# Optimization experiments

Hardware: AMD Instinct MI355X
Metric: run time of the kernel (lower is better)

The kernel has to match this reference:

```python
import jax, jax.numpy as jnp
import numpy as np

D_MODEL = 512
HEADS = 8
CTX = 2048
BATCH = 4
SEQ = 2048


def make_rotary_matrix(context_window, d):
    # Faithful to the source, including theta = 10000 ** (-2*(i-1)/d)
    i = np.arange(d // 2)
    theta = 10000.0 ** (-2.0 * (i - 1) / d)  # [d/2]
    pos = np.arange(context_window)
    m_theta = pos[:, None] * theta[None, :]  # [m, d/2]
    cos, sin = np.cos(m_theta), np.sin(m_theta)
    R = np.zeros((context_window, d, d), dtype=np.float32)
    even, odd = 2 * i, 2 * i + 1
    R[:, even, even] = cos
    R[:, even, odd] = -sin
    R[:, odd, even] = sin
    R[:, odd, odd] = cos
    return jnp.asarray(R)


def setup_inputs() -> dict:
    key = jax.random.key(0)
    ks = jax.random.split(key, 8)
    s = 1.0 / np.sqrt(D_MODEL)
    x = jax.random.normal(ks[0], (BATCH, SEQ, D_MODEL), dtype=jnp.float32)
    Wq = jax.random.normal(ks[1], (D_MODEL, D_MODEL), dtype=jnp.float32) * s
    Wk = jax.random.normal(ks[2], (D_MODEL, D_MODEL), dtype=jnp.float32) * s
    Wv = jax.random.normal(ks[3], (D_MODEL, D_MODEL), dtype=jnp.float32) * s
    in_proj_w = jax.random.normal(ks[4], (3 * D_MODEL, D_MODEL), dtype=jnp.float32) * s
    in_proj_b = jax.random.normal(ks[5], (3 * D_MODEL,), dtype=jnp.float32) * 0.01
    out_w = jax.random.normal(ks[6], (D_MODEL, D_MODEL), dtype=jnp.float32) * s
    out_b = jax.random.normal(ks[7], (D_MODEL,), dtype=jnp.float32) * 0.01
    R = make_rotary_matrix(CTX, D_MODEL)
    return {"x": x, "Wq": Wq, "Wk": Wk, "Wv": Wv, "R": R,
            "in_proj_w": in_proj_w, "in_proj_b": in_proj_b,
            "out_w": out_w, "out_b": out_b}


def reference(x, Wq, Wk, Wv, R, in_proj_w, in_proj_b, out_w, out_b):
    b, m, d = x.shape
    h = HEADS
    hd = d // h
    # outer QKV projections (bias=False)
    q = x @ Wq.T
    k = x @ Wk.T
    v = x @ Wv.T
    # dense per-position rotary rotation: q_out[b,p,:] = q[b,p,:] @ R[p]
    Rm = R[:m]
    q = jnp.einsum('bmd,mde->bme', q, Rm)
    k = jnp.einsum('bmd,mde->bme', k, Rm)
    v = jnp.einsum('bmd,mde->bme', v, Rm)
    # nn.MultiheadAttention in_proj (bias=True) -- dropout skipped (eval)
    wq_i, wk_i, wv_i = jnp.split(in_proj_w, 3, axis=0)
    bq, bk, bv = jnp.split(in_proj_b, 3, axis=0)
    qp = (q @ wq_i.T + bq).reshape(b, m, h, hd).transpose(0, 2, 1, 3)
    kp = (k @ wk_i.T + bk).reshape(b, m, h, hd).transpose(0, 2, 1, 3)
    vp = (v @ wv_i.T + bv).reshape(b, m, h, hd).transpose(0, 2, 1, 3)
    scale = 1.0 / np.sqrt(hd)
    scores = jnp.einsum('bhqd,bhkd->bhqk', qp, kp) * scale
    causal = jnp.triu(jnp.full((m, m), -jnp.inf, dtype=scores.dtype), k=1)
    attn = jax.nn.softmax(scores + causal, axis=-1)
    out = jnp.einsum('bhqk,bhkd->bhqd', attn, vp)
    out = out.transpose(0, 2, 1, 3).reshape(b, m, d)
    return out @ out_w.T + out_b
```

## Files before the change

### kernel.cpp

```cpp
#include <hip/hip_runtime.h>
#include <cmath>

typedef unsigned short u16;
typedef __bf16 bf16x8 __attribute__((ext_vector_type(8)));
typedef float f32x4 __attribute__((ext_vector_type(4)));

#define SEQL 2048
#define NH 8
#define HD 64
#define MROWS 8192

typedef __attribute__((address_space(1))) unsigned int gu32;
typedef __attribute__((address_space(3))) unsigned int lu32;

static __device__ __forceinline__ u16 f2bf(float f) {
  union { float f; unsigned u; } v; v.f = f;
  unsigned u = v.u;
  unsigned r = (u + 0x7FFFu + ((u >> 16) & 1u)) >> 16;
  return (u16)r;
}

static __device__ __forceinline__ void gl16(const u16* g, u16* l) {
  __builtin_amdgcn_global_load_lds((const gu32*)g, (lu32*)l, 16, 0, 0);
}

template<int ROWS>
static __device__ __forceinline__ void stage_tile(const u16* __restrict__ gt, int ld,
                                                  u16* lds, int wid, int lane) {
  int rowl = lane >> 3;
  int coff = ((lane & 7) ^ rowl) * 8;
  #pragma unroll
  for (int t = 0; t < ROWS / 32; ++t) {
    int grp = t * 4 + wid;
    gl16(gt + (size_t)(grp * 8 + rowl) * ld + coff, lds + grp * 512);
  }
}

static __device__ __forceinline__ void cvt4(const float* __restrict__ in,
                                            u16* __restrict__ out, int lb) {
  int i = lb * 1024 + threadIdx.x * 4;
  float4 f = *(const float4*)(in + i);
  ushort4 o;
  o.x = f2bf(f.x); o.y = f2bf(f.y); o.z = f2bf(f.z); o.w = f2bf(f.w);
  *(ushort4*)(out + i) = o;
}

__global__ __launch_bounds__(256) void prep_kernel(
    const float* __restrict__ x,  const float* __restrict__ Wq,
    const float* __restrict__ Wk, const float* __restrict__ Wv,
    const float* __restrict__ ipw, const float* __restrict__ ow,
    u16* __restrict__ xb, u16* __restrict__ Wcatb, u16* __restrict__ ipwb,
    u16* __restrict__ owb, float2* __restrict__ T) {
  int b = blockIdx.x;
  if (b < 4096)      cvt4(x,   xb,                 b);
  else if (b < 4352) cvt4(Wq,  Wcatb,              b - 4096);
  else if (b < 4608) cvt4(Wk,  Wcatb + 262144,     b - 4352);
  else if (b < 4864) cvt4(Wv,  Wcatb + 524288,     b - 4608);
  else if (b < 5632) cvt4(ipw, ipwb,               b - 4864);
  else if (b < 5888) cvt4(ow,  owb,                b - 5632);
  else {
    int idx = (b - 5888) * 256 + threadIdx.x;
    int m = idx >> 8, i = idx & 255;
    double theta = pow(10000.0, -2.0 * ((double)i - 1.0) / 512.0);
    double a = (double)m * theta;
    T[idx] = make_float2((float)cos(a), (float)sin(a));
  }
}

template<int MODE>
__global__ __launch_bounds__(256) void gemm_bt(const u16* __restrict__ A, int lda,
                                               const u16* __restrict__ B, int ldb,
                                               const float* __restrict__ bias,
                                               void* __restrict__ Cv, int ldc,
                                               const float2* __restrict__ T) {
  __shared__ u16 As[128 * 64];
  __shared__ u16 Bs[128 * 64];
  int tid = threadIdx.x;
  int wid = tid >> 6, lane = tid & 63, quad = lane >> 4, l16 = lane & 15;
  int x7 = l16 & 7;
  int m0 = blockIdx.y * 128, n0 = blockIdx.x * 128;
  int wm = (wid >> 1) * 64, wn = (wid & 1) * 64;
  f32x4 acc[4][4] = {};
  for (int kb = 0; kb < 512; kb += 64) {
    stage_tile<128>(A + (size_t)m0 * lda + kb, lda, As, wid, lane);
    stage_tile<128>(B + (size_t)n0 * ldb + kb, ldb, Bs, wid, lane);
    __syncthreads();
    #pragma unroll
    for (int kk = 0; kk < 2; ++kk) {
      int sw = ((kk * 4 + quad) ^ x7) * 8;
      bf16x8 af[4], bfr[4];
      #pragma unroll
      for (int i = 0; i < 4; ++i)
        af[i] = *(const bf16x8*)(&As[(wm + 16 * i + l16) * 64 + sw]);
      #pragma unroll
      for (int j = 0; j < 4; ++j)
        bfr[j] = *(const bf16x8*)(&Bs[(wn + 16 * j + l16) * 64 + sw]);
      #pragma unroll
      for (int i = 0; i < 4; ++i)
        #pragma unroll
        for (int j = 0; j < 4; ++j)
          acc[i][j] = __builtin_amdgcn_mfma_f32_16x16x32_bf16(af[i], bfr[j], acc[i][j], 0, 0, 0);
    }
    __syncthreads();
  }
  float sgn = (l16 & 1) ? -1.f : 1.f;
  #pragma unroll
  for (int i = 0; i < 4; ++i)
    #pragma unroll
    for (int j = 0; j < 4; ++j)
      #pragma unroll
      for (int r = 0; r < 4; ++r) {
        int row = m0 + wm + 16 * i + quad * 4 + r;
        int col = n0 + wn + 16 * j + l16;
        float v = acc[i][j][r];
        if (MODE == 3) {
          float partner = __shfl_xor(v, 1, 64);
          float2 cs = T[(row & 2047) * 256 + ((col & 511) >> 1)];
          v = v * cs.x + sgn * partner * cs.y;
          ((u16*)Cv)[(size_t)row * ldc + col] = f2bf(v);
        } else {
          v += bias[col];
          ((float*)Cv)[(size_t)row * ldc + col] = v;
        }
      }
}

__global__ __launch_bounds__(256) void gemm_inproj(const u16* __restrict__ Aall,
                                                   const u16* __restrict__ B,
                                                   const float* __restrict__ bias,
                                                   u16* __restrict__ qkvh) {
  __shared__ u16 As[128 * 64];
  __shared__ u16 Bs[128 * 64];
  int tid = threadIdx.x;
  int wid = tid >> 6, lane = tid & 63, quad = lane >> 4, l16 = lane & 15;
  int x7 = l16 & 7;
  int m0 = blockIdx.y * 128, n0 = blockIdx.x * 128;
  int qseg = n0 >> 9;
  const u16* A = Aall + qseg * 512;
  int wm = (wid >> 1) * 64, wn = (wid & 1) * 64;
  f32x4 acc[4][4] = {};
  for (int kb = 0; kb < 512; kb += 64) {
    stage_tile<128>(A + (size_t)m0 * 1536 + kb, 1536, As, wid, lane);
    stage_tile<128>(B + (size_t)n0 * 512 + kb, 512, Bs, wid, lane);
    __syncthreads();
    #pragma unroll
    for (int kk = 0; kk < 2; ++kk) {
      int sw = ((kk * 4 + quad) ^ x7) * 8;
      bf16x8 af[4], bfr[4];
      #pragma unroll
      for (int i = 0; i < 4; ++i)
        af[i] = *(const bf16x8*)(&As[(wm + 16 * i + l16) * 64 + sw]);
      #pragma unroll
      for (int j = 0; j < 4; ++j)
        bfr[j] = *(const bf16x8*)(&Bs[(wn + 16 * j + l16) * 64 + sw]);
      #pragma unroll
      for (int i = 0; i < 4; ++i)
        #pragma unroll
        for (int j = 0; j < 4; ++j)
          acc[i][j] = __builtin_amdgcn_mfma_f32_16x16x32_bf16(af[i], bfr[j], acc[i][j], 0, 0, 0);
    }
    __syncthreads();
  }
  #pragma unroll
  for (int i = 0; i < 4; ++i)
    #pragma unroll
    for (int j = 0; j < 4; ++j) {
      int rb = m0 + wm + 16 * i + quad * 4;
      int col = n0 + wn + 16 * j + l16;
      float bv = bias[col];
      int cl = col & 511;
      int h = cl >> 6, dd = cl & 63;
      int bb = rb >> 11;
      if (qseg < 2) {
        #pragma unroll
        for (int r = 0; r < 4; ++r) {
          int mm = (rb + r) & 2047;
          qkvh[(size_t)qseg * MROWS * 512 +
               (((size_t)(bb * NH + h)) * SEQL + mm) * HD + dd] = f2bf(acc[i][j][r] + bv);
        }
      } else {
        ushort4 o;
        o.x = f2bf(acc[i][j][0] + bv); o.y = f2bf(acc[i][j][1] + bv);
        o.z = f2bf(acc[i][j][2] + bv); o.w = f2bf(acc[i][j][3] + bv);
        *(ushort4*)&qkvh[(size_t)2 * MROWS * 512 +
                         ((size_t)(bb * NH + h) * HD + dd) * SEQL + (rb & 2047)] = o;
      }
    }
}

static __device__ __forceinline__ f32x4 mfma_bf16(bf16x8 a, bf16x8 b, f32x4 c) {
  return __builtin_amdgcn_mfma_f32_16x16x32_bf16(a, b, c, 0, 0, 0);
}

static __device__ __forceinline__ void attn_tile(
    bf16x8 qf0, bf16x8 qf1, f32x4* o_acc, float* m_i, float* l_i,
    const u16* Ks, const u16* Vt, u16* Pw, bool diag, int wrow, int quad, int l16) {
  int x7 = l16 & 7;
  int sw0 = (quad ^ x7) * 8;
  int sw1 = ((quad + 4) ^ x7) * 8;
  f32x4 s_acc[4] = {};
  #pragma unroll
  for (int j = 0; j < 4; ++j) {
    bf16x8 bk0 = *(const bf16x8*)(&Ks[(j * 16 + l16) * 64 + sw0]);
    bf16x8 bk1 = *(const bf16x8*)(&Ks[(j * 16 + l16) * 64 + sw1]);
    s_acc[j] = mfma_bf16(qf0, bk0, s_acc[j]);
    s_acc[j] = mfma_bf16(qf1, bk1, s_acc[j]);
  }
  #pragma unroll
  for (int j = 0; j < 4; ++j)
    #pragma unroll
    for (int r = 0; r < 4; ++r) {
      float sv = s_acc[j][r] * 0.125f;
      if (diag && (j * 16 + l16 > wrow + quad * 4 + r)) sv = -__builtin_inff();
      s_acc[j][r] = sv;
    }
  float p[4][4], alpha[4];
  #pragma unroll
  for (int r = 0; r < 4; ++r) {
    float mx = fmaxf(fmaxf(s_acc[0][r], s_acc[1][r]), fmaxf(s_acc[2][r], s_acc[3][r]));
    #pragma unroll
    for (int off = 1; off < 16; off <<= 1) mx = fmaxf(mx, __shfl_xor(mx, off, 64));
    float m_new = fmaxf(m_i[r], mx);
    alpha[r] = __expf(m_i[r] - m_new);
    float rs = 0.f;
    #pragma unroll
    for (int j = 0; j < 4; ++j) { float pv = __expf(s_acc[j][r] - m_new); p[j][r] = pv; rs += pv; }
    #pragma unroll
    for (int off = 1; off < 16; off <<= 1) rs += __shfl_xor(rs, off, 64);
    l_i[r] = l_i[r] * alpha[r] + rs;
    m_i[r] = m_new;
  }
  #pragma unroll
  for (int j = 0; j < 4; ++j)
    #pragma unroll
    for (int r = 0; r < 4; ++r) o_acc[j][r] *= alpha[r];
  #pragma unroll
  for (int j = 0; j < 4; ++j)
    #pragma unroll
    for (int r = 0; r < 4; ++r)
      Pw[(quad * 4 + r) * 80 + j * 16 + l16] = f2bf(p[j][r]);
  bf16x8 pf0 = *(const bf16x8*)(&Pw[l16 * 80 + quad * 8]);
  bf16x8 pf1 = *(const bf16x8*)(&Pw[l16 * 80 + quad * 8 + 32]);
  #pragma unroll
  for (int j = 0; j < 4; ++j) {
    bf16x8 bv0 = *(const bf16x8*)(&Vt[(j * 16 + l16) * 64 + sw0]);
    bf16x8 bv1 = *(const bf16x8*)(&Vt[(j * 16 + l16) * 64 + sw1]);
    o_acc[j] = mfma_bf16(pf0, bv0, o_acc[j]);
    o_acc[j] = mfma_bf16(pf1, bv1, o_acc[j]);
  }
}

__global__ __launch_bounds__(256) void flash_kernel(const u16* __restrict__ Q,
                                                    const u16* __restrict__ K,
                                                    const u16* __restrict__ Vt_g,
                                                    u16* __restrict__ O) {
  __shared__ u16 Ks[64 * 64];
  __shared__ u16 Vt[64 * 64];
  __shared__ u16 Ps[4 * 16 * 80];
  int tid = threadIdx.x;
  int wid = tid >> 6, lane = tid & 63, quad = lane >> 4, l16 = lane & 15;
  int bh = blockIdx.y;
  int b = bh >> 3, h = bh & 7;
  int q0 = blockIdx.x * 128;
  const u16* Qb = Q + (size_t)bh * SEQL * HD;
  const u16* Kb = K + (size_t)bh * SEQL * HD;
  const u16* Vb = Vt_g + (size_t)bh * HD * SEQL;
  u16* Pw = &Ps[wid * 16 * 80];

  int rowA = q0 + wid * 16 + l16;
  int rowB = rowA + 64;
  bf16x8 qA0 = *(const bf16x8*)(Qb + (size_t)rowA * HD + quad * 8);
  bf16x8 qA1 = *(const bf16x8*)(Qb + (size_t)rowA * HD + quad * 8 + 32);
  bf16x8 qB0 = *(const bf16x8*)(Qb + (size_t)rowB * HD + quad * 8);
  bf16x8 qB1 = *(const bf16x8*)(Qb + (size_t)rowB * HD + quad * 8 + 32);

  f32x4 oA[4] = {}, oB[4] = {};
  float mA[4], lA[4], mB[4], lB[4];
  #pragma unroll
  for (int r = 0; r < 4; ++r) {
    mA[r] = -__builtin_inff(); lA[r] = 0.f;
    mB[r] = -__builtin_inff(); lB[r] = 0.f;
  }

  int nkb = q0 / 64 + 2;
  for (int kb = 0; kb < nkb; ++kb) {
    int k0 = kb * 64;
    stage_tile<64>(Kb + (size_t)k0 * HD, HD, Ks, wid, lane);
    stage_tile<64>(Vb + k0, SEQL, Vt, wid, lane);
    __syncthreads();
    if (kb < nkb - 1)
      attn_tile(qA0, qA1, oA, mA, lA, Ks, Vt, Pw, kb == nkb - 2, wid * 16, quad, l16);
    attn_tile(qB0, qB1, oB, mB, lB, Ks, Vt, Pw, kb == nkb - 1, wid * 16, quad, l16);
    __syncthreads();
  }
  #pragma unroll
  for (int j = 0; j < 4; ++j)
    #pragma unroll
    for (int r = 0; r < 4; ++r) {
      int mA_idx = q0 + wid * 16 + quad * 4 + r;
      O[((size_t)(b * SEQL + mA_idx)) * 512 + h * HD + j * 16 + l16] = f2bf(oA[j][r] / lA[r]);
      int mB_idx = mA_idx + 64;
      O[((size_t)(b * SEQL + mB_idx)) * 512 + h * HD + j * 16 + l16] = f2bf(oB[j][r] / lB[r]);
    }
}

extern "C" void kernel_launch(void* const* d_in, const int* in_sizes, int n_in,
                              void* d_out, int out_size, void* d_ws, size_t ws_size,
                              hipStream_t stream) {
  const float* x   = (const float*)d_in[0];
  const float* Wq  = (const float*)d_in[1];
  const float* Wk  = (const float*)d_in[2];
  const float* Wv  = (const float*)d_in[3];
  const float* ipw = (const float*)d_in[5];
  const float* ipb = (const float*)d_in[6];
  const float* ow  = (const float*)d_in[7];
  const float* ob  = (const float*)d_in[8];
  float* out = (float*)d_out;

  char* w = (char*)d_ws;
  auto alloc = [&](size_t bytes) { void* p = w; w += bytes; return p; };
  u16* xb    = (u16*)alloc(8192UL * 512 * 2);
  u16* Wcatb = (u16*)alloc(3UL * 512 * 512 * 2);
  u16* ipwb  = (u16*)alloc(1536UL * 512 * 2);
  u16* owb   = (u16*)alloc(512UL * 512 * 2);
  u16* QKV0  = (u16*)alloc(8192UL * 1536 * 2);
  u16* qkvh  = (u16*)alloc(3UL * 8192 * 512 * 2);
  u16* Ob    = (u16*)alloc(8192UL * 512 * 2);
  float2* T  = (float2*)alloc(2048UL * 256 * sizeof(float2));

  prep_kernel<<<7936, 256, 0, stream>>>(x, Wq, Wk, Wv, ipw, ow,
                                        xb, Wcatb, ipwb, owb, T);
  gemm_bt<3><<<dim3(12, 64), 256, 0, stream>>>(xb, 512, Wcatb, 512, nullptr,
                                               QKV0, 1536, T);
  gemm_inproj<<<dim3(12, 64), 256, 0, stream>>>(QKV0, ipwb, ipb, qkvh);
  flash_kernel<<<dim3(16, 32), 256, 0, stream>>>(
      qkvh, qkvh + 8192UL * 512, qkvh + 2UL * 8192 * 512, Ob);
  gemm_bt<2><<<dim3(4, 64), 256, 0, stream>>>(Ob, 512, owb, 512, ob, out, 512, nullptr);
}
```

Before: 2.508 ms.

## Stage 128-key K/V tiles per iteration and swizzle the P scratch buffer

The flash attention loop now stages 128 keys of K and V^T per iteration instead of 64, and processes them as two 64-key chunks for each of the two query row groups. This halves the number of barrier pairs and staging rounds per block. The P write/read pattern in LDS now uses an XOR swizzle to reduce bank conflicts, and V^T gets a new 128-wide swizzled layout. LDS use grows, which could lower occupancy.

```diff
diff --git a/kernel.cpp b/kernel.cpp
--- a/kernel.cpp
+++ b/kernel.cpp
@@ -33,6 +33,18 @@
   for (int t = 0; t < ROWS / 32; ++t) {
     int grp = t * 4 + wid;
     gl16(gt + (size_t)(grp * 8 + rowl) * ld + coff, lds + grp * 512);
+  }
+}
+
+static __device__ __forceinline__ void stage_vt128(const u16* __restrict__ Vb, int k0,
+                                                   u16* Vt, int wid, int lane) {
+  int rowl = lane >> 4;
+  int cl = lane & 15;
+  #pragma unroll
+  for (int t = 0; t < 4; ++t) {
+    int grp = t * 4 + wid;
+    int row = grp * 4 + rowl;
+    gl16(Vb + (size_t)row * SEQL + k0 + (cl ^ (row & 15)) * 8, Vt + grp * 512);
   }
 }
 
@@ -192,17 +204,17 @@
   return __builtin_amdgcn_mfma_f32_16x16x32_bf16(a, b, c, 0, 0, 0);
 }
 
-static __device__ __forceinline__ void attn_tile(
+static __device__ __forceinline__ void attn_chunk(
     bf16x8 qf0, bf16x8 qf1, f32x4* o_acc, float* m_i, float* l_i,
-    const u16* Ks, const u16* Vt, u16* Pw, bool diag, int wrow, int quad, int l16) {
+    const u16* Ks, const u16* Vt, u16* Pw, int c, bool diag,
+    int wrow, int quad, int l16) {
   int x7 = l16 & 7;
-  int sw0 = (quad ^ x7) * 8;
-  int sw1 = ((quad + 4) ^ x7) * 8;
   f32x4 s_acc[4] = {};
   #pragma unroll
   for (int j = 0; j < 4; ++j) {
-    bf16x8 bk0 = *(const bf16x8*)(&Ks[(j * 16 + l16) * 64 + sw0]);
-    bf16x8 bk1 = *(const bf16x8*)(&Ks[(j * 16 + l16) * 64 + sw1]);
+    int krow = c * 64 + j * 16 + l16;
+    bf16x8 bk0 = *(const bf16x8*)(&Ks[krow * 64 + ((quad ^ x7) * 8)]);
+    bf16x8 bk1 = *(const bf16x8*)(&Ks[krow * 64 + (((quad + 4) ^ x7) * 8)]);
     s_acc[j] = mfma_bf16(qf0, bk0, s_acc[j]);
     s_acc[j] = mfma_bf16(qf1, bk1, s_acc[j]);
   }
@@ -237,14 +249,18 @@
   #pragma unroll
   for (int j = 0; j < 4; ++j)
     #pragma unroll
-    for (int r = 0; r < 4; ++r)
-      Pw[(quad * 4 + r) * 80 + j * 16 + l16] = f2bf(p[j][r]);
-  bf16x8 pf0 = *(const bf16x8*)(&Pw[l16 * 80 + quad * 8]);
-  bf16x8 pf1 = *(const bf16x8*)(&Pw[l16 * 80 + quad * 8 + 32]);
+    for (int r = 0; r < 4; ++r) {
+      int rr = quad * 4 + r;
+      int chunk = j * 2 + (l16 >> 3);
+      Pw[rr * 80 + ((chunk ^ (rr & 7)) * 8) + (l16 & 7)] = f2bf(p[j][r]);
+    }
+  bf16x8 pf0 = *(const bf16x8*)(&Pw[l16 * 80 + ((quad ^ x7) * 8)]);
+  bf16x8 pf1 = *(const bf16x8*)(&Pw[l16 * 80 + (((quad + 4) ^ x7) * 8)]);
   #pragma unroll
   for (int j = 0; j < 4; ++j) {
-    bf16x8 bv0 = *(const bf16x8*)(&Vt[(j * 16 + l16) * 64 + sw0]);
-    bf16x8 bv1 = *(const bf16x8*)(&Vt[(j * 16 + l16) * 64 + sw1]);
+    int vrow = j * 16 + l16;
+    bf16x8 bv0 = *(const bf16x8*)(&Vt[vrow * 128 + (((c * 8 + quad) ^ l16) * 8)]);
+    bf16x8 bv1 = *(const bf16x8*)(&Vt[vrow * 128 + (((c * 8 + 4 + quad) ^ l16) * 8)]);
     o_acc[j] = mfma_bf16(pf0, bv0, o_acc[j]);
     o_acc[j] = mfma_bf16(pf1, bv1, o_acc[j]);
   }
@@ -254,8 +270,8 @@
                                                     const u16* __restrict__ K,
                                                     const u16* __restrict__ Vt_g,
                                                     u16* __restrict__ O) {
-  __shared__ u16 Ks[64 * 64];
-  __shared__ u16 Vt[64 * 64];
+  __shared__ u16 Ks[128 * 64];
+  __shared__ u16 Vt[64 * 128];
   __shared__ u16 Ps[4 * 16 * 80];
   int tid = threadIdx.x;
   int wid = tid >> 6, lane = tid & 63, quad = lane >> 4, l16 = lane & 15;
@@ -282,15 +298,18 @@
     mB[r] = -__builtin_inff(); lB[r] = 0.f;
   }
 
-  int nkb = q0 / 64 + 2;
-  for (int kb = 0; kb < nkb; ++kb) {
-    int k0 = kb * 64;
-    stage_tile<64>(Kb + (size_t)k0 * HD, HD, Ks, wid, lane);
-    stage_tile<64>(Vb + k0, SEQL, Vt, wid, lane);
-    __syncthreads();
-    if (kb < nkb - 1)
-      attn_tile(qA0, qA1, oA, mA, lA, Ks, Vt, Pw, kb == nkb - 2, wid * 16, quad, l16);
-    attn_tile(qB0, qB1, oB, mB, lB, Ks, Vt, Pw, kb == nkb - 1, wid * 16, quad, l16);
+  int T = q0 / 128 + 1;
+  for (int t = 0; t < T; ++t) {
+    int k0 = t * 128;
+    stage_tile<128>(Kb + (size_t)k0 * HD, HD, Ks, wid, lane);
+    stage_vt128(Vb, k0, Vt, wid, lane);
+    __syncthreads();
+    bool last = (t == T - 1);
+    attn_chunk(qA0, qA1, oA, mA, lA, Ks, Vt, Pw, 0, last, wid * 16, quad, l16);
+    if (!last)
+      attn_chunk(qA0, qA1, oA, mA, lA, Ks, Vt, Pw, 1, false, wid * 16, quad, l16);
+    attn_chunk(qB0, qB1, oB, mB, lB, Ks, Vt, Pw, 0, false, wid * 16, quad, l16);
+    attn_chunk(qB0, qB1, oB, mB, lB, Ks, Vt, Pw, 1, last, wid * 16, quad, l16);
     __syncthreads();
   }
   #pragma unroll
```

Result: slower. 2.586 ms (+3.1%).
